# Performance work log

Measured on AMD Instinct MI355X. Metric: run time of the kernel, lower is better.

## Reference

```python
import jax, jax.numpy as jnp
import numpy as np

B, S, D, H = 2, 2048, 1024, 16
DEPTH = D // H
NEG = -1e9

def setup_inputs() -> dict:
    key = jax.random.key(0)
    k = jax.random.split(key, 4)
    return {
        "token_inputs": jax.random.normal(k[0], (B, S, D), dtype=jnp.float32),
        "mask": jnp.zeros((B, 1, 1, S), dtype=jnp.float32),
        "W_qkv": jax.random.normal(k[1], (D, 3 * D), dtype=jnp.float32) * 0.02,
        "b_qkv": jnp.zeros((3 * D,), dtype=jnp.float32),
        "W_out": jax.random.normal(k[2], (D, D), dtype=jnp.float32) * 0.02,
        "b_out": jnp.zeros((D,), dtype=jnp.float32),
    }

def reference(token_inputs, mask, W_qkv, b_qkv, W_out, b_out):
    # fused QKV projection
    qkv = token_inputs @ W_qkv + b_qkv                       # [B,S,3D]
    q, k, v = jnp.split(qkv, 3, axis=-1)                     # [B,S,D] each
    # split heads -> [B,H,S,depth]
    split = lambda x: x.reshape(B, S, H, DEPTH).transpose(0, 2, 1, 3)
    q, k, v = split(q), split(k), split(v)
    # causal additive mask: 0 on/below diagonal, -1e9 above
    causal = (1.0 - jnp.tril(jnp.ones((S, S), dtype=jnp.float32))) * NEG
    full_mask = mask + causal                                # [B,1,S,S]
    # scaled dot-product attention
    scores = jnp.einsum('bhqd,bhkd->bhqk', q, k) / jnp.sqrt(jnp.float32(DEPTH))
    scores = scores + full_mask
    attn = jax.nn.softmax(scores, axis=-1)                   # [B,H,S,S]
    ctx = jnp.einsum('bhqk,bhkd->bhqd', attn, v)             # [B,H,S,depth]
    # merge heads and final projection
    ctx = ctx.transpose(0, 2, 1, 3).reshape(B, S, D)
    return ctx @ W_out + b_out
```

## Files before the change

kernel.cpp:

```cpp
#include <hip/hip_runtime.h>
#include <hip/hip_bf16.h>

#define B_ 2
#define S_ 2048
#define D_ 1024
#define H_ 16
#define DEPTH_ 64

typedef __attribute__((ext_vector_type(4))) float f32x4;
typedef __attribute__((ext_vector_type(16))) float f32x16;
typedef __attribute__((ext_vector_type(8))) short bf16x8;
typedef const __attribute__((address_space(1))) unsigned int gu32;
typedef __attribute__((address_space(3))) unsigned int lu32;

__device__ __forceinline__ void gload_lds16(const void* g, void* l) {
  __builtin_amdgcn_global_load_lds((gu32*)g, (lu32*)l, 16, 0, 0);
}

__device__ __forceinline__ short f2bf(float f) {
  union { float f; unsigned u; } v; v.f = f;
  return (short)((v.u + 0x7FFFu + ((v.u >> 16) & 1u)) >> 16);
}
__device__ __forceinline__ unsigned pk2(float lo, float hi) {
  return ((unsigned)(unsigned short)f2bf(hi) << 16) | (unsigned short)f2bf(lo);
}

__global__ __launch_bounds__(256) void cast_kernel(const float* __restrict__ in,
                                                   short* __restrict__ out, int n4) {
  int i = blockIdx.x * 256 + threadIdx.x;
  if (i < n4) {
    const float4 v = reinterpret_cast<const float4*>(in)[i];
    short4 o;
    o.x = f2bf(v.x); o.y = f2bf(v.y); o.z = f2bf(v.z); o.w = f2bf(v.w);
    reinterpret_cast<short4*>(out)[i] = o;
  }
}

__global__ __launch_bounds__(256) void transpose_cast_kernel(const float* __restrict__ W,
                                                             short* __restrict__ WT,
                                                             int K, int N) {
  __shared__ short tile[32][33];
  int n0 = blockIdx.x * 32, k0 = blockIdx.y * 32;
  int tx = threadIdx.x, ty = threadIdx.y;
#pragma unroll
  for (int j = 0; j < 4; ++j)
    tile[ty + 8 * j][tx] = f2bf(W[(size_t)(k0 + ty + 8 * j) * N + n0 + tx]);
  __syncthreads();
#pragma unroll
  for (int j = 0; j < 4; ++j)
    WT[(size_t)(n0 + ty + 8 * j) * K + k0 + tx] = tile[tx][ty + 8 * j];
}

template <int EPI, int BM>
__global__ __launch_bounds__(512) void gemm_bt_kernel(
    const short* __restrict__ A, const short* __restrict__ BT,
    const float* __restrict__ bias,
    short* __restrict__ Qh, short* __restrict__ Kh, short* __restrict__ VTt,
    float* __restrict__ Out, int M, int N, int K) {
  constexpr int MI = BM / 64;
  constexpr int ASZ = BM * 32;
  constexpr int BSZ = 128 * 32;
  __shared__ short smem[2 * ASZ + 2 * BSZ];
  const int bm = blockIdx.y * BM, bn = blockIdx.x * 128;
  const int tid = threadIdx.x;
  const int w = tid >> 6, lane = tid & 63;
  const int wr = w >> 1, wc = w & 1;
  const int lr = lane & 15, lg = lane >> 4;
  const int s_r = lane >> 2, s_c = (lane & 3) * 8;
  f32x4 acc[MI][4] = {};
  const int nk = K >> 5;

  auto stage = [&](int buf, int kt) {
    short* Asb = smem + (buf ? ASZ : 0);
    short* Bsb = smem + 2 * ASZ + (buf ? BSZ : 0);
    if (BM == 128 || w < 4)
      gload_lds16(&A[(size_t)(bm + 16 * w + s_r) * K + kt * 32 + s_c], &Asb[16 * w * 32]);
    gload_lds16(&BT[(size_t)(bn + 16 * w + s_r) * K + kt * 32 + s_c], &Bsb[16 * w * 32]);
  };

  stage(0, 0);
  __syncthreads();
  int cur = 0;
  for (int kt = 0; kt < nk; ++kt) {
    if (kt + 1 < nk) stage(cur ^ 1, kt + 1);
    const short* Asb = smem + (cur ? ASZ : 0);
    const short* Bsb = smem + 2 * ASZ + (cur ? BSZ : 0);
    bf16x8 af[MI], bfr[4];
#pragma unroll
    for (int mi = 0; mi < MI; ++mi)
      af[mi] = *reinterpret_cast<const bf16x8*>(&Asb[((BM / 4) * wr + 16 * mi + lr) * 32 + 8 * lg]);
#pragma unroll
    for (int ni = 0; ni < 4; ++ni)
      bfr[ni] = *reinterpret_cast<const bf16x8*>(&Bsb[(64 * wc + 16 * ni + lr) * 32 + 8 * lg]);
#pragma unroll
    for (int mi = 0; mi < MI; ++mi)
#pragma unroll
      for (int ni = 0; ni < 4; ++ni)
        acc[mi][ni] = __builtin_amdgcn_mfma_f32_16x16x32_bf16(af[mi], bfr[ni], acc[mi][ni], 0, 0, 0);
    __syncthreads();
    cur ^= 1;
  }

  if constexpr (EPI == 0) {
    if (bn >= 2 * D_) {
      __syncthreads();
      short* vt = smem;
#pragma unroll
      for (int mi = 0; mi < MI; ++mi)
#pragma unroll
        for (int ni = 0; ni < 4; ++ni)
#pragma unroll
          for (int r = 0; r < 4; r += 2) {
            int row_local = (BM / 4) * wr + 16 * mi + 4 * lg + r;
            int col_local = 64 * wc + 16 * ni + lr;
            float bv = bias[bn + col_local];
            unsigned u = pk2(acc[mi][ni][r] + bv, acc[mi][ni][r + 1] + bv);
            int rsw = row_local ^ ((col_local & 7) << 3);
            *reinterpret_cast<unsigned*>(&vt[col_local * 128 + rsw]) = u;
          }
      __syncthreads();
      const int b = bm >> 11, sbase = bm & (S_ - 1);
#pragma unroll
      for (int p = 0; p < 4; ++p) {
        int slot = 512 * p + tid;
        int vrow = slot >> 4, seg = slot & 15;
        int dd_col = bn - 2 * D_ + vrow;
        int hh = dd_col >> 6, dd = dd_col & 63;
        int csw = (seg * 8) ^ ((vrow & 7) << 3);
        short* dst = &VTt[((size_t)(b * H_ + hh) * DEPTH_ + dd) * S_ + sbase + seg * 8];
        *reinterpret_cast<bf16x8*>(dst) = *reinterpret_cast<const bf16x8*>(&vt[vrow * 128 + csw]);
      }
    } else {
#pragma unroll
      for (int mi = 0; mi < MI; ++mi)
#pragma unroll
        for (int ni = 0; ni < 4; ++ni)
#pragma unroll
          for (int r = 0; r < 4; ++r) {
            int row = bm + (BM / 4) * wr + 16 * mi + 4 * lg + r;
            int col = bn + 64 * wc + 16 * ni + lr;
            float v = acc[mi][ni][r] + bias[col];
            int b = row >> 11, s = row & (S_ - 1);
            int which = col >> 10, cm = col & (D_ - 1);
            int hh = cm >> 6, dd = cm & 63;
            short bv = f2bf(v);
            size_t bh = (size_t)(b * H_ + hh);
            if (which == 0) Qh[(bh * S_ + s) * DEPTH_ + dd] = bv;
            else            Kh[(bh * S_ + s) * DEPTH_ + dd] = bv;
          }
    }
  } else {
#pragma unroll
    for (int mi = 0; mi < MI; ++mi)
#pragma unroll
      for (int ni = 0; ni < 4; ++ni)
#pragma unroll
        for (int r = 0; r < 4; ++r) {
          int row = bm + (BM / 4) * wr + 16 * mi + 4 * lg + r;
          int col = bn + 64 * wc + 16 * ni + lr;
          Out[(size_t)row * N + col] = acc[mi][ni][r] + bias[col];
        }
  }
}

__global__ __launch_bounds__(256, 4) void attn_kernel(
    const short* __restrict__ Qh, const short* __restrict__ Kh,
    const short* __restrict__ VTt, const float* __restrict__ mask,
    short* __restrict__ ctx) {
  constexpr float SC = 0.125f * 1.44269504f;
  __shared__ short smem[16384];
  const int bid = blockIdx.x;
  const int qt = 31 - (bid >> 5);
  const int bh = bid & 31;
  const int b = bh >> 4, h = bh & 15;
  const short* Qp = Qh + (size_t)bh * S_ * DEPTH_;
  const short* Kp = Kh + (size_t)bh * S_ * DEPTH_;
  const short* Vp = VTt + (size_t)bh * DEPTH_ * S_;
  const int tid = threadIdx.x;
  const int w = tid >> 6, lane = tid & 63;
  const int sw = w & 1, ch = w >> 1;
  const int lq = lane & 31, hi = lane >> 5;
  const int q0w = qt * 64 + sw * 32;
  const int scs = 8 * ((lane & 7) ^ ((lane >> 3) & 7));
  const int srw = lane >> 3;
  short* Ksc = smem + ch * 8192;
  short* Vsc = Ksc + 4096;

  bf16x8 qf[4];
#pragma unroll
  for (int ksd = 0; ksd < 4; ++ksd)
    qf[ksd] = *reinterpret_cast<const bf16x8*>(&Qp[(size_t)(q0w + lq) * DEPTH_ + 16 * ksd + 8 * hi]);

  bf16x8 ones = {};
  if (hi == 0) ones[0] = (short)0x3F80;

  f32x16 acc0 = {}, acc1 = {};
  float m_run = -1e30f, l_run = 0.f;

  const int nt = qt + 1;
  const int nh = (nt + 1) >> 1;
  for (int i = 0; i < nh; ++i) {
    const int kt = ch ? (nh + i) : i;
    const bool valid = kt < nt;
    const int k0 = kt * 64;
    __syncthreads();
    if (valid) {
#pragma unroll
      for (int j = 0; j < 4; ++j) {
        const int brow = sw * 32 + j * 8;
        gload_lds16(&Kp[(size_t)(k0 + brow + srw) * DEPTH_ + scs], &Ksc[brow * 64]);
        gload_lds16(&Vp[(size_t)(brow + srw) * S_ + k0 + scs], &Vsc[brow * 64]);
      }
    }
    __syncthreads();
    if (!valid) continue;

    f32x16 sc[2] = {{}, {}};
#pragma unroll
    for (int h2 = 0; h2 < 2; ++h2) {
#pragma unroll
      for (int ksd = 0; ksd < 4; ++ksd) {
        const int row = h2 * 32 + lq;
        const int col = (16 * ksd + 8 * hi) ^ ((row & 7) * 8);
        bf16x8 kf = *reinterpret_cast<const bf16x8*>(&Ksc[row * 64 + col]);
        sc[h2] = __builtin_amdgcn_mfma_f32_32x32x16_bf16(kf, qf[ksd], sc[h2], 0, 0, 0);
      }
      float mv = mask[(size_t)b * S_ + k0 + h2 * 32 + lq];
      bf16x8 maf = {};
      if (hi == 0) maf[0] = f2bf(8.f * mv);
      sc[h2] = __builtin_amdgcn_mfma_f32_32x32x16_bf16(maf, ones, sc[h2], 0, 0, 0);
    }
    if (kt == nt - 1) {
      const int qg = q0w + lq;
#pragma unroll
      for (int h2 = 0; h2 < 2; ++h2)
#pragma unroll
        for (int r = 0; r < 16; ++r) {
          int kvg = k0 + (r & 3) + 8 * (r >> 2) + 4 * hi + 32 * h2;
          if (kvg > qg) sc[h2][r] = -1e30f;
        }
    }
    float mx = sc[0][0];
#pragma unroll
    for (int r = 1; r < 16; ++r) mx = fmaxf(mx, sc[0][r]);
#pragma unroll
    for (int r = 0; r < 16; ++r) mx = fmaxf(mx, sc[1][r]);
    mx = fmaxf(mx, __shfl_xor(mx, 32));
    const float m_tile = mx * SC;
    const float m_new = fmaxf(m_run, m_tile);
    const float corr = exp2f(m_run - m_new);
    m_run = m_new;
    float su = 0.f;
#pragma unroll
    for (int h2 = 0; h2 < 2; ++h2)
#pragma unroll
      for (int r = 0; r < 16; ++r) {
        float p = exp2f(fmaf(sc[h2][r], SC, -m_new));
        sc[h2][r] = p;
        su += p;
      }
    su += __shfl_xor(su, 32);
    l_run = l_run * corr + su;
#pragma unroll
    for (int r = 0; r < 16; ++r) { acc0[r] *= corr; acc1[r] *= corr; }

#pragma unroll
    for (int h2 = 0; h2 < 2; ++h2) {
#pragma unroll
      for (int ks = 0; ks < 2; ++ks) {
        const int rb = 8 * ks;
        unsigned a = pk2(sc[h2][rb + 0], sc[h2][rb + 1]);
        unsigned bq = pk2(sc[h2][rb + 2], sc[h2][rb + 3]);
        unsigned c = pk2(sc[h2][rb + 4], sc[h2][rb + 5]);
        unsigned d = pk2(sc[h2][rb + 6], sc[h2][rb + 7]);
        unsigned sa = __shfl_xor((int)a, 32), sb = __shfl_xor((int)bq, 32);
        unsigned sx = __shfl_xor((int)c, 32), sy = __shfl_xor((int)d, 32);
        union { unsigned u[4]; bf16x8 v; } pf;
        pf.u[0] = hi ? sx : a;
        pf.u[1] = hi ? sy : bq;
        pf.u[2] = hi ? c : sa;
        pf.u[3] = hi ? d : sb;
#pragma unroll
        for (int dh = 0; dh < 2; ++dh) {
          const int row = dh * 32 + lq;
          const int col = (32 * h2 + 16 * ks + 8 * hi) ^ ((row & 7) * 8);
          bf16x8 vf = *reinterpret_cast<const bf16x8*>(&Vsc[row * 64 + col]);
          if (dh == 0) acc0 = __builtin_amdgcn_mfma_f32_32x32x16_bf16(vf, pf.v, acc0, 0, 0, 0);
          else         acc1 = __builtin_amdgcn_mfma_f32_32x32x16_bf16(vf, pf.v, acc1, 0, 0, 0);
        }
      }
    }
  }

  __syncthreads();
  float* F  = (float*)smem;
  float* ML = (float*)(smem + 8192);
  short* ob = smem + 8704;
  if (ch == 1) {
    float* dst = F + ((size_t)sw * 64 + lane) * 32;
#pragma unroll
    for (int r = 0; r < 16; ++r) { dst[r] = acc0[r]; dst[16 + r] = acc1[r]; }
    ML[(sw * 64 + lane) * 2 + 0] = m_run;
    ML[(sw * 64 + lane) * 2 + 1] = l_run;
  }
  __syncthreads();
  if (ch == 0) {
    const float* src = F + ((size_t)sw * 64 + lane) * 32;
    const float m1 = ML[(sw * 64 + lane) * 2 + 0];
    const float l1 = ML[(sw * 64 + lane) * 2 + 1];
    const float mM = fmaxf(m_run, m1);
    const float f0 = exp2f(m_run - mM), f1 = exp2f(m1 - mM);
    const float rl = 1.f / (l_run * f0 + l1 * f1);
    const float g0 = f0 * rl, g1 = f1 * rl;
#pragma unroll
    for (int r = 0; r < 16; ++r) {
      acc0[r] = acc0[r] * g0 + src[r] * g1;
      acc1[r] = acc1[r] * g0 + src[16 + r] * g1;
    }
#pragma unroll
    for (int dh = 0; dh < 2; ++dh) {
      const f32x16& Aa = dh ? acc1 : acc0;
#pragma unroll
      for (int g = 0; g < 4; ++g)
#pragma unroll
        for (int p = 0; p < 2; ++p) {
          int r0 = 4 * g + 2 * p;
          int d0 = 2 * p + 8 * g + 4 * hi + 32 * dh;
          unsigned u = pk2(Aa[r0], Aa[r0 + 1]);
          *reinterpret_cast<unsigned*>(&ob[(sw * 32 + lq) * 72 + d0]) = u;
        }
    }
  }
  __syncthreads();
  {
    const int row = tid >> 2, seg = tid & 3;
    short* dst = ctx + ((size_t)b * S_ + qt * 64 + row) * D_ + h * 64 + seg * 16;
    const short* srcp = &ob[row * 72 + seg * 16];
    *reinterpret_cast<bf16x8*>(dst) = *reinterpret_cast<const bf16x8*>(srcp);
    *reinterpret_cast<bf16x8*>(dst + 8) = *reinterpret_cast<const bf16x8*>(srcp + 8);
  }
}

extern "C" void kernel_launch(void* const* d_in, const int* in_sizes, int n_in,
                              void* d_out, int out_size, void* d_ws, size_t ws_size,
                              hipStream_t stream) {
  const float* X    = (const float*)d_in[0];
  const float* mask = (const float*)d_in[1];
  const float* Wqkv = (const float*)d_in[2];
  const float* bqkv = (const float*)d_in[3];
  const float* Wout = (const float*)d_in[4];
  const float* bout = (const float*)d_in[5];
  float* Out = (float*)d_out;

  short* ws    = (short*)d_ws;
  short* Xb    = ws;
  short* WqkvT = Xb + (size_t)4096 * 1024;
  short* WoutT = WqkvT + (size_t)3072 * 1024;
  short* Qh    = WoutT + (size_t)1024 * 1024;
  short* Kh    = Qh + (size_t)B_ * H_ * S_ * DEPTH_;
  short* VTt   = Kh + (size_t)B_ * H_ * S_ * DEPTH_;
  short* ctx   = VTt + (size_t)B_ * H_ * S_ * DEPTH_;

  cast_kernel<<<4096, 256, 0, stream>>>(X, Xb, (4096 * 1024) / 4);
  transpose_cast_kernel<<<dim3(96, 32), dim3(32, 8), 0, stream>>>(Wqkv, WqkvT, 1024, 3072);
  transpose_cast_kernel<<<dim3(32, 32), dim3(32, 8), 0, stream>>>(Wout, WoutT, 1024, 1024);
  gemm_bt_kernel<0, 128><<<dim3(24, 32), 512, 0, stream>>>(Xb, WqkvT, bqkv, Qh, Kh, VTt, nullptr,
                                                           4096, 3072, 1024);
  attn_kernel<<<1024, 256, 0, stream>>>(Qh, Kh, VTt, mask, ctx);
  gemm_bt_kernel<1, 64><<<dim3(8, 64), 512, 0, stream>>>(ctx, WoutT, bout, nullptr, nullptr, nullptr,
                                                         Out, 4096, 1024, 1024);
}
```

Measured before the change: 123.9 us.

## Use hardware bf16 pack, interleave query-tile order, and lazily rescale softmax

Replaces the software round-to-nearest bf16 pack with the v_cvt_pk_bf16_f32 instruction in the cast and attention kernels. It also reorders the causal query-tile schedule so blocks alternate heavy and light tiles, aiming to balance load across CUs. The online softmax now rescales the accumulators only when some lane's tile max exceeds the running max by more than 8 (log2 units), which skips the correction multiplies on most iterations. The lazy rescale lets the unnormalized probabilities grow up to 2^8 before bf16 packing, which slightly changes the numerics.

```diff
diff --git a/kernel.cpp b/kernel.cpp
--- a/kernel.cpp
+++ b/kernel.cpp
@@ -22,7 +22,9 @@
   return (short)((v.u + 0x7FFFu + ((v.u >> 16) & 1u)) >> 16);
 }
 __device__ __forceinline__ unsigned pk2(float lo, float hi) {
-  return ((unsigned)(unsigned short)f2bf(hi) << 16) | (unsigned short)f2bf(lo);
+  unsigned r;
+  asm("v_cvt_pk_bf16_f32 %0, %1, %2" : "=v"(r) : "v"(lo), "v"(hi));
+  return r;
 }
 
 __global__ __launch_bounds__(256) void cast_kernel(const float* __restrict__ in,
@@ -30,9 +32,10 @@
   int i = blockIdx.x * 256 + threadIdx.x;
   if (i < n4) {
     const float4 v = reinterpret_cast<const float4*>(in)[i];
-    short4 o;
-    o.x = f2bf(v.x); o.y = f2bf(v.y); o.z = f2bf(v.z); o.w = f2bf(v.w);
-    reinterpret_cast<short4*>(out)[i] = o;
+    short2 a, b;
+    *reinterpret_cast<unsigned*>(&a) = pk2(v.x, v.y);
+    *reinterpret_cast<unsigned*>(&b) = pk2(v.z, v.w);
+    reinterpret_cast<short4*>(out)[i] = make_short4(a.x, a.y, b.x, b.y);
   }
 }
 
@@ -170,7 +173,8 @@
   constexpr float SC = 0.125f * 1.44269504f;
   __shared__ short smem[16384];
   const int bid = blockIdx.x;
-  const int qt = 31 - (bid >> 5);
+  const int j = bid >> 5, g = j & 7, rr = j >> 3;
+  const int qt = (rr == 0) ? 31 - g : (rr == 1) ? 16 + g : (rr == 2) ? 15 - g : g;
   const int bh = bid & 31;
   const int b = bh >> 4, h = bh & 15;
   const short* Qp = Qh + (size_t)bh * S_ * DEPTH_;
@@ -206,8 +210,8 @@
     __syncthreads();
     if (valid) {
 #pragma unroll
-      for (int j = 0; j < 4; ++j) {
-        const int brow = sw * 32 + j * 8;
+      for (int jj = 0; jj < 4; ++jj) {
+        const int brow = sw * 32 + jj * 8;
         gload_lds16(&Kp[(size_t)(k0 + brow + srw) * DEPTH_ + scs], &Ksc[brow * 64]);
         gload_lds16(&Vp[(size_t)(brow + srw) * S_ + k0 + scs], &Vsc[brow * 64]);
       }
@@ -240,29 +244,32 @@
           if (kvg > qg) sc[h2][r] = -1e30f;
         }
     }
-    float mx = sc[0][0];
-#pragma unroll
-    for (int r = 1; r < 16; ++r) mx = fmaxf(mx, sc[0][r]);
+    float mx = fmaxf(sc[0][0], sc[0][1]);
+#pragma unroll
+    for (int r = 2; r < 16; ++r) mx = fmaxf(mx, sc[0][r]);
 #pragma unroll
     for (int r = 0; r < 16; ++r) mx = fmaxf(mx, sc[1][r]);
     mx = fmaxf(mx, __shfl_xor(mx, 32));
     const float m_tile = mx * SC;
-    const float m_new = fmaxf(m_run, m_tile);
-    const float corr = exp2f(m_run - m_new);
-    m_run = m_new;
+    if (__any(m_tile > m_run + 8.f)) {
+      const float m_new = fmaxf(m_run, m_tile);
+      const float corr = exp2f(m_run - m_new);
+      m_run = m_new;
+      l_run *= corr;
+#pragma unroll
+      for (int r = 0; r < 16; ++r) { acc0[r] *= corr; acc1[r] *= corr; }
+    }
     float su = 0.f;
 #pragma unroll
     for (int h2 = 0; h2 < 2; ++h2)
 #pragma unroll
       for (int r = 0; r < 16; ++r) {
-        float p = exp2f(fmaf(sc[h2][r], SC, -m_new));
+        float p = exp2f(fmaf(sc[h2][r], SC, -m_run));
         sc[h2][r] = p;
         su += p;
       }
     su += __shfl_xor(su, 32);
-    l_run = l_run * corr + su;
-#pragma unroll
-    for (int r = 0; r < 16; ++r) { acc0[r] *= corr; acc1[r] *= corr; }
+    l_run += su;
 
 #pragma unroll
     for (int h2 = 0; h2 < 2; ++h2) {
@@ -321,11 +328,11 @@
     for (int dh = 0; dh < 2; ++dh) {
       const f32x16& Aa = dh ? acc1 : acc0;
 #pragma unroll
-      for (int g = 0; g < 4; ++g)
+      for (int gg = 0; gg < 4; ++gg)
 #pragma unroll
         for (int p = 0; p < 2; ++p) {
-          int r0 = 4 * g + 2 * p;
-          int d0 = 2 * p + 8 * g + 4 * hi + 32 * dh;
+          int r0 = 4 * gg + 2 * p;
+          int d0 = 2 * p + 8 * gg + 4 * hi + 32 * dh;
           unsigned u = pk2(Aa[r0], Aa[r0 + 1]);
           *reinterpret_cast<unsigned*>(&ob[(sw * 32 + lq) * 72 + d0]) = u;
         }
```

After: 116.8 us. 1.06x faster.
